# Kernel tuning notes

Measured on AMD Instinct MI355X. Metric: run time of the kernel, lower is better.

## Reference

```python
import jax, jax.numpy as jnp
import numpy as np

T, B, D = 256, 64, 512


def setup_inputs() -> dict:
    key = jax.random.key(0)
    ks = jax.random.split(key, 9)
    s = 1.0 / np.sqrt(D)  # torch Linear default init scale (uniform), use scaled normal
    return {
        "x": jax.random.normal(ks[0], (T, B, D), dtype=jnp.float32),
        "y": jax.random.normal(ks[1], (T, B, D), dtype=jnp.float32),
        "Wr": jax.random.normal(ks[2], (D, D), dtype=jnp.float32) * s,
        "Ur": jax.random.normal(ks[3], (D, D), dtype=jnp.float32) * s,
        "Wz": jax.random.normal(ks[4], (D, D), dtype=jnp.float32) * s,
        "Uz": jax.random.normal(ks[5], (D, D), dtype=jnp.float32) * s,
        "Wg": jax.random.normal(ks[6], (D, D), dtype=jnp.float32) * s,
        "Ug": jax.random.normal(ks[7], (D, D), dtype=jnp.float32) * s,
        "bg": jnp.full((D,), 2.0, dtype=jnp.float32),
    }


def reference(x, y, Wr, Ur, Wz, Uz, Wg, Ug, bg):
    # GTrXL gating unit. torch Linear(y) == y @ W.T
    r = jax.nn.sigmoid(jnp.einsum("tbd,ed->tbe", y, Wr) + jnp.einsum("tbd,ed->tbe", x, Ur))
    z = jax.nn.sigmoid(jnp.einsum("tbd,ed->tbe", y, Wz) + jnp.einsum("tbd,ed->tbe", x, Uz) - bg)
    h = jnp.tanh(jnp.einsum("tbd,ed->tbe", y, Wg) + jnp.einsum("tbd,ed->tbe", r * x, Ug))
    g = (1.0 - z) * x + z * h  # (T, B, D)
    return g
```

## Files before the change

kernel.cpp:

```cpp
#include <hip/hip_runtime.h>
#include <stdint.h>

typedef unsigned short u16;
typedef __attribute__((ext_vector_type(8))) __bf16 bf16x8;
typedef __attribute__((ext_vector_type(4))) float f32x4;

#define Dn 512
#define Mn 16384


__device__ __forceinline__ u16 f2bf(float f) {
  unsigned u = __float_as_uint(f);
  u += 0x7fffu + ((u >> 16) & 1u);
  return (u16)(u >> 16);
}

__device__ __forceinline__ float bf2f(u16 b) {
  return __uint_as_float(((unsigned)b) << 16);
}

__device__ __forceinline__ void async16(const u16* g, u16* l) {
  __builtin_amdgcn_global_load_lds(
      (const __attribute__((address_space(1))) unsigned int*)g,
      (__attribute__((address_space(3))) unsigned int*)l, 16, 0, 0);
}

__device__ __forceinline__ float sigmoidf_(float v) {
  return 1.f / (1.f + __expf(-v));
}

__global__ void cast_all(const float* __restrict__ y, const float* __restrict__ x,
                         const float* w0, const float* w1, const float* w2,
                         const float* w3, const float* w4, const float* w5,
                         u16* __restrict__ yb, u16* __restrict__ xb,
                         u16* __restrict__ wb) {
  int b = blockIdx.x;
  const float* src;
  u16* dst;
  if (b < 8192) {
    src = y; dst = yb;
  } else if (b < 16384) {
    src = x; dst = xb; b -= 8192;
  } else {
    b -= 16384;
    const int wi = b >> 8;
    b &= 255;
    src = wi == 0 ? w0 : wi == 1 ? w1 : wi == 2 ? w2 : wi == 3 ? w3 : wi == 4 ? w4 : w5;
    dst = wb + wi * 262144;
  }
  const int i4 = b * 256 + (int)threadIdx.x;
  float4 v = ((const float4*)src)[i4];
  ushort4 o;
  o.x = f2bf(v.x); o.y = f2bf(v.y); o.z = f2bf(v.z); o.w = f2bf(v.w);
  ((ushort4*)dst)[i4] = o;
}

__global__ __launch_bounds__(256, 2) void gemm_rz(
    const u16* __restrict__ yb, const u16* __restrict__ xb,
    const u16* __restrict__ wb,
    const float* __restrict__ bg,
    u16* __restrict__ rxb, u16* __restrict__ zb) {
  __shared__ u16 sY[128 * 64];
  __shared__ u16 sX[128 * 64];
  __shared__ u16 sW[4 * 64 * 64];

  const int tid = threadIdx.x;
  const int lane = tid & 63;
  const int wave = tid >> 6;
  const int waveM = wave >> 1, waveN = wave & 1;
  const int nb = blockIdx.x & 7, mb = blockIdx.x >> 3;
  const int rowStart = mb * 128, colStart = nb * 64;
  const int rbase = tid >> 3;
  const int cbase = (tid & 7) * 8;
  const int wbyte = (tid & 192) * 16;
  const int lm = lane & 15, quad = lane >> 4;

  f32x4 accR[4][2] = {};
  f32x4 accZ[4][2] = {};

  for (int k0 = 0; k0 < Dn; k0 += 64) {
#pragma unroll
    for (int s = 0; s < 4; ++s) {
      async16(yb + (size_t)(rowStart + s * 32 + rbase) * Dn + k0 + cbase,
              (u16*)((char*)sY + s * 4096 + wbyte));
      async16(xb + (size_t)(rowStart + s * 32 + rbase) * Dn + k0 + cbase,
              (u16*)((char*)sX + s * 4096 + wbyte));
    }
#pragma unroll
    for (int w = 0; w < 4; ++w)
#pragma unroll
      for (int s = 0; s < 2; ++s)
        async16(wb + (size_t)w * 262144 +
                    (size_t)(colStart + s * 32 + rbase) * Dn + k0 + cbase,
                (u16*)((char*)sW + w * 8192 + s * 4096 + wbyte));
    __syncthreads();

#pragma unroll
    for (int kk = 0; kk < 2; ++kk) {
      bf16x8 ay[4], ax[4], bw[4][2];
#pragma unroll
      for (int i = 0; i < 4; ++i) {
        const int off = (waveM * 64 + i * 16 + lm) * 64 + kk * 32 + quad * 8;
        ay[i] = *(const bf16x8*)(sY + off);
        ax[i] = *(const bf16x8*)(sX + off);
      }
#pragma unroll
      for (int w = 0; w < 4; ++w)
#pragma unroll
        for (int j = 0; j < 2; ++j)
          bw[w][j] = *(const bf16x8*)(sW + w * 4096 +
                                      (waveN * 32 + j * 16 + lm) * 64 + kk * 32 + quad * 8);
#pragma unroll
      for (int i = 0; i < 4; ++i)
#pragma unroll
        for (int j = 0; j < 2; ++j) {
          accR[i][j] = __builtin_amdgcn_mfma_f32_16x16x32_bf16(ay[i], bw[0][j], accR[i][j], 0, 0, 0);
          accR[i][j] = __builtin_amdgcn_mfma_f32_16x16x32_bf16(ax[i], bw[1][j], accR[i][j], 0, 0, 0);
          accZ[i][j] = __builtin_amdgcn_mfma_f32_16x16x32_bf16(ay[i], bw[2][j], accZ[i][j], 0, 0, 0);
          accZ[i][j] = __builtin_amdgcn_mfma_f32_16x16x32_bf16(ax[i], bw[3][j], accZ[i][j], 0, 0, 0);
        }
    }
    __syncthreads();
  }

#pragma unroll
  for (int j = 0; j < 2; ++j) {
    const int e = colStart + waveN * 32 + j * 16 + lm;
    const float bgv = bg[e];
#pragma unroll
    for (int i = 0; i < 4; ++i) {
      const int m0 = rowStart + waveM * 64 + i * 16 + quad * 4;
#pragma unroll
      for (int rg = 0; rg < 4; ++rg) {
        const size_t idx = (size_t)(m0 + rg) * Dn + e;
        const float r = sigmoidf_(accR[i][j][rg]);
        rxb[idx] = f2bf(r * bf2f(xb[idx]));
        zb[idx] = f2bf(sigmoidf_(accZ[i][j][rg] - bgv));
      }
    }
  }
}

__global__ __launch_bounds__(256, 2) void gemm_gu(
    const u16* __restrict__ yb, const u16* __restrict__ rxb,
    const u16* __restrict__ wg,
    const u16* __restrict__ zb, const u16* __restrict__ xb,
    float* __restrict__ out) {
  __shared__ u16 sA[128 * 64];
  __shared__ u16 sW[64 * 64];

  const int tid = threadIdx.x;
  const int lane = tid & 63;
  const int wave = tid >> 6;
  const int waveM = wave >> 1, waveN = wave & 1;
  const int nb = blockIdx.x & 7, mb = blockIdx.x >> 3;
  const int rowStart = mb * 128, colStart = nb * 64;
  const int rbase = tid >> 3;
  const int cbase = (tid & 7) * 8;
  const int wbyte = (tid & 192) * 16;
  const int lm = lane & 15, quad = lane >> 4;

  f32x4 acc[4][2] = {};

  for (int kq = 0; kq < 16; ++kq) {
    const int half = kq >> 3;
    const int k0 = (kq & 7) * 64;
    const u16* abase = half ? rxb : yb;
    const u16* wbase = wg + (size_t)half * 262144;
#pragma unroll
    for (int s = 0; s < 4; ++s)
      async16(abase + (size_t)(rowStart + s * 32 + rbase) * Dn + k0 + cbase,
              (u16*)((char*)sA + s * 4096 + wbyte));
#pragma unroll
    for (int s = 0; s < 2; ++s)
      async16(wbase + (size_t)(colStart + s * 32 + rbase) * Dn + k0 + cbase,
              (u16*)((char*)sW + s * 4096 + wbyte));
    __syncthreads();

#pragma unroll
    for (int kk = 0; kk < 2; ++kk) {
      bf16x8 aa[4], bw[2];
#pragma unroll
      for (int i = 0; i < 4; ++i)
        aa[i] = *(const bf16x8*)(sA + (waveM * 64 + i * 16 + lm) * 64 + kk * 32 + quad * 8);
#pragma unroll
      for (int j = 0; j < 2; ++j)
        bw[j] = *(const bf16x8*)(sW + (waveN * 32 + j * 16 + lm) * 64 + kk * 32 + quad * 8);
#pragma unroll
      for (int i = 0; i < 4; ++i)
#pragma unroll
        for (int j = 0; j < 2; ++j)
          acc[i][j] = __builtin_amdgcn_mfma_f32_16x16x32_bf16(aa[i], bw[j], acc[i][j], 0, 0, 0);
    }
    __syncthreads();
  }

#pragma unroll
  for (int j = 0; j < 2; ++j) {
    const int e = colStart + waveN * 32 + j * 16 + lm;
#pragma unroll
    for (int i = 0; i < 4; ++i) {
      const int m0 = rowStart + waveM * 64 + i * 16 + quad * 4;
#pragma unroll
      for (int rg = 0; rg < 4; ++rg) {
        const size_t idx = (size_t)(m0 + rg) * Dn + e;
        const float pre = acc[i][j][rg];
        const float ex = __expf(-2.f * pre);
        const float h = (1.f - ex) / (1.f + ex);
        const float z = bf2f(zb[idx]);
        const float xv = bf2f(xb[idx]);
        out[idx] = (1.f - z) * xv + z * h;
      }
    }
  }
}

extern "C" void kernel_launch(void* const* d_in, const int* in_sizes, int n_in,
                              void* d_out, int out_size, void* d_ws, size_t ws_size,
                              hipStream_t stream) {
  const float* x  = (const float*)d_in[0];
  const float* y  = (const float*)d_in[1];
  const float* Wr = (const float*)d_in[2];
  const float* Ur = (const float*)d_in[3];
  const float* Wz = (const float*)d_in[4];
  const float* Uz = (const float*)d_in[5];
  const float* Wg = (const float*)d_in[6];
  const float* Ug = (const float*)d_in[7];
  const float* bg = (const float*)d_in[8];
  float* out = (float*)d_out;

  char* ws = (char*)d_ws;
  u16* yb  = (u16*)(ws);
  u16* xb  = (u16*)(ws + 16777216);
  u16* rxb = (u16*)(ws + 2 * 16777216);
  u16* wb  = (u16*)(ws + 3 * 16777216);
  u16* zb  = (u16*)(ws + 3 * 16777216 + 3145728);

  cast_all<<<17920, 256, 0, stream>>>(y, x, Wr, Ur, Wz, Uz, Wg, Ug, yb, xb, wb);
  gemm_rz<<<1024, 256, 0, stream>>>(yb, xb, wb, bg, rxb, zb);
  gemm_gu<<<1024, 256, 0, stream>>>(yb, rxb, wb + (size_t)4 * 262144, zb, xb, out);
}
```

Before: 224.3 us.

## Widen GEMM tiles to 128x128 and XOR-swizzle LDS layout

Both GEMM kernels now compute 128x128 output tiles instead of 128x64, which halves the grid and doubles accumulators per wave so each loaded A tile is reused across more columns. gemm_rz moves to a K step of 32, and it stages its weight fragments one matrix at a time to limit register pressure. Both kernels apply an XOR swizzle to the LDS column index on the async global-to-LDS writes and the fragment reads, aiming to remove bank conflicts. The risks are higher VGPR use from 32 accumulators in gemm_rz, which may reduce occupancy, and a smaller grid of 512 blocks that may not fill all compute units evenly.

New measurement: 214.7 us. 1.04x faster.

```diff
diff --git a/kernel.cpp b/kernel.cpp
--- a/kernel.cpp
+++ b/kernel.cpp
@@ -60,30 +60,34 @@
     const u16* __restrict__ wb,
     const float* __restrict__ bg,
     u16* __restrict__ rxb, u16* __restrict__ zb) {
-  __shared__ u16 sY[128 * 64];
-  __shared__ u16 sX[128 * 64];
-  __shared__ u16 sW[4 * 64 * 64];
+  __shared__ u16 smem[24576];
+  u16* sY = smem;
+  u16* sX = smem + 4096;
+  u16* sW = smem + 8192;
 
   const int tid = threadIdx.x;
   const int lane = tid & 63;
   const int wave = tid >> 6;
   const int waveM = wave >> 1, waveN = wave & 1;
-  const int nb = blockIdx.x & 7, mb = blockIdx.x >> 3;
-  const int rowStart = mb * 128, colStart = nb * 64;
-  const int rbase = tid >> 3;
-  const int cbase = (tid & 7) * 8;
+  const int mb = blockIdx.x >> 2, nb = blockIdx.x & 3;
+  const int rowStart = mb * 128, colStart = nb * 128;
   const int wbyte = (tid & 192) * 16;
   const int lm = lane & 15, quad = lane >> 4;
 
-  f32x4 accR[4][2] = {};
-  f32x4 accZ[4][2] = {};
-
-  for (int k0 = 0; k0 < Dn; k0 += 64) {
-#pragma unroll
-    for (int s = 0; s < 4; ++s) {
-      async16(yb + (size_t)(rowStart + s * 32 + rbase) * Dn + k0 + cbase,
+  const int srow = tid >> 2;
+  const int scol = (((tid & 3) ^ ((tid >> 3) & 3)) * 8);
+
+  const int aswz = (quad ^ ((lm >> 1) & 3)) * 8;
+
+  f32x4 accR[4][4] = {};
+  f32x4 accZ[4][4] = {};
+
+  for (int k0 = 0; k0 < Dn; k0 += 32) {
+#pragma unroll
+    for (int s = 0; s < 2; ++s) {
+      async16(yb + (size_t)(rowStart + s * 64 + srow) * Dn + k0 + scol,
               (u16*)((char*)sY + s * 4096 + wbyte));
-      async16(xb + (size_t)(rowStart + s * 32 + rbase) * Dn + k0 + cbase,
+      async16(xb + (size_t)(rowStart + s * 64 + srow) * Dn + k0 + scol,
               (u16*)((char*)sX + s * 4096 + wbyte));
     }
 #pragma unroll
@@ -91,41 +95,55 @@
 #pragma unroll
       for (int s = 0; s < 2; ++s)
         async16(wb + (size_t)w * 262144 +
-                    (size_t)(colStart + s * 32 + rbase) * Dn + k0 + cbase,
+                    (size_t)(colStart + s * 64 + srow) * Dn + k0 + scol,
                 (u16*)((char*)sW + w * 8192 + s * 4096 + wbyte));
     __syncthreads();
 
-#pragma unroll
-    for (int kk = 0; kk < 2; ++kk) {
-      bf16x8 ay[4], ax[4], bw[4][2];
-#pragma unroll
-      for (int i = 0; i < 4; ++i) {
-        const int off = (waveM * 64 + i * 16 + lm) * 64 + kk * 32 + quad * 8;
-        ay[i] = *(const bf16x8*)(sY + off);
-        ax[i] = *(const bf16x8*)(sX + off);
-      }
-#pragma unroll
-      for (int w = 0; w < 4; ++w)
-#pragma unroll
-        for (int j = 0; j < 2; ++j)
-          bw[w][j] = *(const bf16x8*)(sW + w * 4096 +
-                                      (waveN * 32 + j * 16 + lm) * 64 + kk * 32 + quad * 8);
-#pragma unroll
-      for (int i = 0; i < 4; ++i)
-#pragma unroll
-        for (int j = 0; j < 2; ++j) {
-          accR[i][j] = __builtin_amdgcn_mfma_f32_16x16x32_bf16(ay[i], bw[0][j], accR[i][j], 0, 0, 0);
-          accR[i][j] = __builtin_amdgcn_mfma_f32_16x16x32_bf16(ax[i], bw[1][j], accR[i][j], 0, 0, 0);
-          accZ[i][j] = __builtin_amdgcn_mfma_f32_16x16x32_bf16(ay[i], bw[2][j], accZ[i][j], 0, 0, 0);
-          accZ[i][j] = __builtin_amdgcn_mfma_f32_16x16x32_bf16(ax[i], bw[3][j], accZ[i][j], 0, 0, 0);
-        }
-    }
-    __syncthreads();
-  }
-
-#pragma unroll
-  for (int j = 0; j < 2; ++j) {
-    const int e = colStart + waveN * 32 + j * 16 + lm;
+    bf16x8 ay[4], ax[4], bw[4];
+#pragma unroll
+    for (int i = 0; i < 4; ++i) {
+      const int off = (waveM * 64 + i * 16 + lm) * 32 + aswz;
+      ay[i] = *(const bf16x8*)(sY + off);
+      ax[i] = *(const bf16x8*)(sX + off);
+    }
+#pragma unroll
+    for (int j = 0; j < 4; ++j)
+      bw[j] = *(const bf16x8*)(sW + 0 * 4096 + (waveN * 64 + j * 16 + lm) * 32 + aswz);
+#pragma unroll
+    for (int i = 0; i < 4; ++i)
+#pragma unroll
+      for (int j = 0; j < 4; ++j)
+        accR[i][j] = __builtin_amdgcn_mfma_f32_16x16x32_bf16(ay[i], bw[j], accR[i][j], 0, 0, 0);
+#pragma unroll
+    for (int j = 0; j < 4; ++j)
+      bw[j] = *(const bf16x8*)(sW + 1 * 4096 + (waveN * 64 + j * 16 + lm) * 32 + aswz);
+#pragma unroll
+    for (int i = 0; i < 4; ++i)
+#pragma unroll
+      for (int j = 0; j < 4; ++j)
+        accR[i][j] = __builtin_amdgcn_mfma_f32_16x16x32_bf16(ax[i], bw[j], accR[i][j], 0, 0, 0);
+#pragma unroll
+    for (int j = 0; j < 4; ++j)
+      bw[j] = *(const bf16x8*)(sW + 2 * 4096 + (waveN * 64 + j * 16 + lm) * 32 + aswz);
+#pragma unroll
+    for (int i = 0; i < 4; ++i)
+#pragma unroll
+      for (int j = 0; j < 4; ++j)
+        accZ[i][j] = __builtin_amdgcn_mfma_f32_16x16x32_bf16(ay[i], bw[j], accZ[i][j], 0, 0, 0);
+#pragma unroll
+    for (int j = 0; j < 4; ++j)
+      bw[j] = *(const bf16x8*)(sW + 3 * 4096 + (waveN * 64 + j * 16 + lm) * 32 + aswz);
+#pragma unroll
+    for (int i = 0; i < 4; ++i)
+#pragma unroll
+      for (int j = 0; j < 4; ++j)
+        accZ[i][j] = __builtin_amdgcn_mfma_f32_16x16x32_bf16(ax[i], bw[j], accZ[i][j], 0, 0, 0);
+    __syncthreads();
+  }
+
+#pragma unroll
+  for (int j = 0; j < 4; ++j) {
+    const int e = colStart + waveN * 64 + j * 16 + lm;
     const float bgv = bg[e];
 #pragma unroll
     for (int i = 0; i < 4; ++i) {
@@ -146,21 +164,24 @@
     const u16* __restrict__ wg,
     const u16* __restrict__ zb, const u16* __restrict__ xb,
     float* __restrict__ out) {
-  __shared__ u16 sA[128 * 64];
-  __shared__ u16 sW[64 * 64];
+  __shared__ u16 smem[16384];
+  u16* sA = smem;
+  u16* sB = smem + 8192;
 
   const int tid = threadIdx.x;
   const int lane = tid & 63;
   const int wave = tid >> 6;
   const int waveM = wave >> 1, waveN = wave & 1;
-  const int nb = blockIdx.x & 7, mb = blockIdx.x >> 3;
-  const int rowStart = mb * 128, colStart = nb * 64;
-  const int rbase = tid >> 3;
-  const int cbase = (tid & 7) * 8;
+  const int mb = blockIdx.x >> 2, nb = blockIdx.x & 3;
+  const int rowStart = mb * 128, colStart = nb * 128;
   const int wbyte = (tid & 192) * 16;
   const int lm = lane & 15, quad = lane >> 4;
 
-  f32x4 acc[4][2] = {};
+  const int srow = tid >> 3;
+  const int scol = (((tid & 7) ^ ((tid >> 3) & 7)) * 8);
+  const int lswz = lm & 7;
+
+  f32x4 acc[4][4] = {};
 
   for (int kq = 0; kq < 16; ++kq) {
     const int half = kq >> 3;
@@ -168,36 +189,37 @@
     const u16* abase = half ? rxb : yb;
     const u16* wbase = wg + (size_t)half * 262144;
 #pragma unroll
-    for (int s = 0; s < 4; ++s)
-      async16(abase + (size_t)(rowStart + s * 32 + rbase) * Dn + k0 + cbase,
+    for (int s = 0; s < 4; ++s) {
+      async16(abase + (size_t)(rowStart + s * 32 + srow) * Dn + k0 + scol,
               (u16*)((char*)sA + s * 4096 + wbyte));
-#pragma unroll
-    for (int s = 0; s < 2; ++s)
-      async16(wbase + (size_t)(colStart + s * 32 + rbase) * Dn + k0 + cbase,
-              (u16*)((char*)sW + s * 4096 + wbyte));
+      async16(wbase + (size_t)(colStart + s * 32 + srow) * Dn + k0 + scol,
+              (u16*)((char*)sB + s * 4096 + wbyte));
+    }
     __syncthreads();
 
 #pragma unroll
     for (int kk = 0; kk < 2; ++kk) {
-      bf16x8 aa[4], bw[2];
+      bf16x8 aa[4], bw[4];
 #pragma unroll
       for (int i = 0; i < 4; ++i)
-        aa[i] = *(const bf16x8*)(sA + (waveM * 64 + i * 16 + lm) * 64 + kk * 32 + quad * 8);
-#pragma unroll
-      for (int j = 0; j < 2; ++j)
-        bw[j] = *(const bf16x8*)(sW + (waveN * 32 + j * 16 + lm) * 64 + kk * 32 + quad * 8);
+        aa[i] = *(const bf16x8*)(sA + (waveM * 64 + i * 16 + lm) * 64 +
+                                 ((kk * 4 + quad) ^ lswz) * 8);
+#pragma unroll
+      for (int j = 0; j < 4; ++j)
+        bw[j] = *(const bf16x8*)(sB + (waveN * 64 + j * 16 + lm) * 64 +
+                                 ((kk * 4 + quad) ^ lswz) * 8);
 #pragma unroll
       for (int i = 0; i < 4; ++i)
 #pragma unroll
-        for (int j = 0; j < 2; ++j)
+        for (int j = 0; j < 4; ++j)
           acc[i][j] = __builtin_amdgcn_mfma_f32_16x16x32_bf16(aa[i], bw[j], acc[i][j], 0, 0, 0);
     }
     __syncthreads();
   }
 
 #pragma unroll
-  for (int j = 0; j < 2; ++j) {
-    const int e = colStart + waveN * 32 + j * 16 + lm;
+  for (int j = 0; j < 4; ++j) {
+    const int e = colStart + waveN * 64 + j * 16 + lm;
 #pragma unroll
     for (int i = 0; i < 4; ++i) {
       const int m0 = rowStart + waveM * 64 + i * 16 + quad * 4;
@@ -237,6 +259,6 @@
   u16* zb  = (u16*)(ws + 3 * 16777216 + 3145728);
 
   cast_all<<<17920, 256, 0, stream>>>(y, x, Wr, Ur, Wz, Uz, Wg, Ug, yb, xb, wb);
-  gemm_rz<<<1024, 256, 0, stream>>>(yb, xb, wb, bg, rxb, zb);
-  gemm_gu<<<1024, 256, 0, stream>>>(yb, rxb, wb + (size_t)4 * 262144, zb, xb, out);
-}
+  gemm_rz<<<512, 256, 0, stream>>>(yb, xb, wb, bg, rxb, zb);
+  gemm_gu<<<512, 256, 0, stream>>>(yb, rxb, wb + (size_t)4 * 262144, zb, xb, out);
+}
```
